# Kernel optimization log

Measured on AMD Instinct MI355X. Metric: run time of the kernel, lower is better.

## Reference

```python
import jax, jax.numpy as jnp
import numpy as np

B, C_IN, C_OUT, H, W, K = 8, 32, 32, 96, 96, 5


def setup_inputs() -> dict:
    key = jax.random.key(0)
    k1, k2 = jax.random.split(key)
    f = jax.random.normal(k1, (B, C_IN, H, W), dtype=jnp.float32)
    # xavier_uniform-style init for the structuring element h
    fan_in = C_IN * K * K
    fan_out = C_OUT * K * K
    bound = float(np.sqrt(6.0 / (fan_in + fan_out)))
    h = jax.random.uniform(k2, (C_OUT, C_IN, K, K), dtype=jnp.float32,
                           minval=-bound, maxval=bound)
    return {"f": f, "h": h}


def reference(f, h):
    """Morphological max-plus dilation with 'same' padding.

    out[b,o,y,x] = max_{c,i,j} f[b,c,y+i-p, x+j-p] + h[o,c,i,j]
    """
    b, c, hh, ww = f.shape
    o, _, k, _ = h.shape
    p = k // 2
    neg = -jnp.finfo(f.dtype).max / 2
    fp = jnp.pad(f, ((0, 0), (0, 0), (p, p), (p, p)), constant_values=neg)
    out = jnp.full((b, o, hh, ww), neg, dtype=f.dtype)
    for i in range(k):          # fixed small kernel loop (k*k = 25 taps)
        for j in range(k):
            sl = fp[:, :, i:i + hh, j:j + ww]              # (B, C, H, W)
            w_ij = h[:, :, i, j]                            # (O, C)
            # max-plus over input channels: (B,1,C,H,W) + (O,C,1,1)
            cand = jnp.max(sl[:, None] + w_ij[None, :, :, None, None], axis=2)
            out = jnp.maximum(out, cand)
    return out
```

## Files before the change

kernel.cpp:

```cpp
#include <hip/hip_runtime.h>


#define B_ 8
#define C_ 32
#define O_ 32
#define H_ 96
#define W_ 96
#define K_ 5
#define KK_ (K_ * K_)

#define TX_ 24
#define RT_ 4
#define CS_ 4
#define TY_ (RT_ * CS_)
#define NT_ (TX_ * TY_)
#define XR_ 4
#define OP_ 2
#define OB_ (OP_ * 2)
#define CG_ (C_ / CS_)

#define PH_ 100
#define PW_ 104
#define PLSZ_ (PH_ * PW_)
#define FPAD_BYTES ((size_t)B_ * C_ * PLSZ_ * 4)

#define NEGF (-30000.0f)

typedef _Float16 h2 __attribute__((ext_vector_type(2)));

static __device__ __forceinline__ h2 h2b(unsigned u) {
    return __builtin_bit_cast(h2, u);
}
static __device__ __forceinline__ unsigned bh2(h2 v) {
    return __builtin_bit_cast(unsigned, v);
}

__global__ __launch_bounds__(256)
void prepad_kernel(const float* __restrict__ f, unsigned* __restrict__ fpad) {
    const int idx = blockIdx.x * 256 + threadIdx.x;
    const int c = blockIdx.y;
    const int b = blockIdx.z;
    if (idx >= PLSZ_) return;
    const int row = idx / PW_;
    const int col = idx - row * PW_;
    const int y = row - 2;
    const int x = col - 2;
    float v = NEGF;
    if ((unsigned)y < H_ && (unsigned)x < W_)
        v = f[((size_t)(b * C_ + c) * H_ + y) * W_ + x];
    _Float16 hv = (_Float16)v;
    h2 d; d.x = hv; d.y = hv;
    fpad[(size_t)(b * C_ + c) * PLSZ_ + idx] = bh2(d);
}

template <bool PADDED>
__global__ __launch_bounds__(NT_)
void dilate_main(const unsigned* __restrict__ fpad,
                 const float* __restrict__ f,
                 const float* __restrict__ h, float* __restrict__ out) {
    const int tx  = threadIdx.x;
    const int ty  = threadIdx.y;
    const int tid = ty * TX_ + tx;
    const int ry  = ty & (RT_ - 1);
    const int g   = ty >> 2;

    const int ytile = blockIdx.x;
    const int og    = blockIdx.y;
    const int b     = blockIdx.z;
    const int y0 = ytile * RT_;
    const int o0 = og * OB_;
    const int x0 = XR_ * tx;
    const int yb = y0 + ry;

    __shared__ unsigned hs2[C_][64];
    __shared__ unsigned comb[CS_ - 1][OP_ * XR_][RT_ * TX_];

    for (int idx = tid; idx < C_ * KK_ * OP_; idx += NT_) {
        int c  = idx / (KK_ * OP_);
        int rr = idx - c * (KK_ * OP_);
        int ij = rr / OP_;
        int op = rr - ij * OP_;
        int o  = o0 + 2 * op;
        float a0 = h[((size_t)o * C_ + c) * KK_ + ij];
        float a1 = h[((size_t)(o + 1) * C_ + c) * KK_ + ij];
        h2 p; p.x = (_Float16)a0; p.y = (_Float16)a1;
        hs2[c][ij * OP_ + op] = bh2(p);
    }
    __syncthreads();

    h2 acc[OP_][XR_];
    {
        h2 neg; neg.x = (_Float16)NEGF; neg.y = (_Float16)NEGF;
#pragma unroll
        for (int op = 0; op < OP_; ++op)
#pragma unroll
            for (int xx = 0; xx < XR_; ++xx) acc[op][xx] = neg;
    }

    const int c0 = g * CG_;
    for (int cc = 0; cc < CG_; ++cc) {
        const int c = c0 + cc;

        unsigned win[K_][8];
        if (PADDED) {
            const unsigned* p =
                fpad + (size_t)(b * C_ + c) * PLSZ_ + yb * PW_ + x0;
#pragma unroll
            for (int i = 0; i < K_; ++i) {
                const uint4* q = (const uint4*)(p + i * PW_);
                uint4 w0 = q[0];
                uint4 w1 = q[1];
                win[i][0] = w0.x; win[i][1] = w0.y;
                win[i][2] = w0.z; win[i][3] = w0.w;
                win[i][4] = w1.x; win[i][5] = w1.y;
                win[i][6] = w1.z; win[i][7] = w1.w;
            }
        } else {
            const float* fc = f + (size_t)(b * C_ + c) * (H_ * W_);
#pragma unroll
            for (int i = 0; i < K_; ++i) {
#pragma unroll
                for (int q = 0; q < 8; ++q) {
                    int yy = yb + i - 2;
                    int xc = x0 - 2 + q;
                    bool ok = ((unsigned)yy < H_) && ((unsigned)xc < W_);
                    float v = ok ? fc[(size_t)yy * W_ + xc] : NEGF;
                    _Float16 hv = (_Float16)v;
                    h2 d; d.x = hv; d.y = hv;
                    win[i][q] = bh2(d);
                }
            }
        }

        unsigned hu[2 * KK_];
        {
            const uint4* hsrc = (const uint4*)&hs2[c][0];
#pragma unroll
            for (int k = 0; k < 12; ++k) {
                uint4 v = hsrc[k];
                hu[4 * k]     = v.x;
                hu[4 * k + 1] = v.y;
                hu[4 * k + 2] = v.z;
                hu[4 * k + 3] = v.w;
            }
            uint2 hd = *(const uint2*)&hs2[c][48];
            hu[48] = hd.x;
            hu[49] = hd.y;
        }

#pragma unroll
        for (int n = 0; n < 2 * KK_; ++n) asm volatile("" : "+v"(hu[n]));
#pragma unroll
        for (int i = 0; i < K_; ++i)
#pragma unroll
            for (int q = 0; q < 8; ++q) asm volatile("" : "+v"(win[i][q]));

#pragma unroll
        for (int i = 0; i < K_; ++i) {
#pragma unroll
            for (int j = 0; j < K_; ++j) {
                h2 h0 = h2b(hu[(i * K_ + j) * OP_]);
                h2 h1 = h2b(hu[(i * K_ + j) * OP_ + 1]);
#pragma unroll
                for (int xx = 0; xx < XR_; ++xx) {
                    h2 fv = h2b(win[i][xx + j]);
                    acc[0][xx] = __builtin_elementwise_max(acc[0][xx], fv + h0);
                    acc[1][xx] = __builtin_elementwise_max(acc[1][xx], fv + h1);
                }
            }
        }
    }

    const int t96 = ry * TX_ + tx;
    if (g > 0) {
#pragma unroll
        for (int op = 0; op < OP_; ++op)
#pragma unroll
            for (int xx = 0; xx < XR_; ++xx)
                comb[g - 1][op * XR_ + xx][t96] = bh2(acc[op][xx]);
    }
    __syncthreads();
    if (g == 0) {
#pragma unroll
        for (int op = 0; op < OP_; ++op)
#pragma unroll
            for (int xx = 0; xx < XR_; ++xx) {
                const int row = op * XR_ + xx;
                h2 v0 = h2b(comb[0][row][t96]);
                h2 v1 = h2b(comb[1][row][t96]);
                h2 v2 = h2b(comb[2][row][t96]);
                h2 m = __builtin_elementwise_max(v0, v1);
                m = __builtin_elementwise_max(m, v2);
                acc[op][xx] = __builtin_elementwise_max(acc[op][xx], m);
            }

        const int y = yb;
#pragma unroll
        for (int op = 0; op < OP_; ++op) {
            const int o = o0 + 2 * op;
            float4 lo = make_float4((float)acc[op][0].x, (float)acc[op][1].x,
                                    (float)acc[op][2].x, (float)acc[op][3].x);
            float4 hi = make_float4((float)acc[op][0].y, (float)acc[op][1].y,
                                    (float)acc[op][2].y, (float)acc[op][3].y);
            *(float4*)&out[(((size_t)b * O_ + o)     * H_ + y) * W_ + x0] = lo;
            *(float4*)&out[(((size_t)b * O_ + o + 1) * H_ + y) * W_ + x0] = hi;
        }
    }
}

extern "C" void kernel_launch(void* const* d_in, const int* in_sizes, int n_in,
                              void* d_out, int out_size, void* d_ws, size_t ws_size,
                              hipStream_t stream) {
    const float* f = (const float*)d_in[0];
    const float* h = (const float*)d_in[1];
    float* out = (float*)d_out;

    dim3 mgrid(H_ / RT_, O_ / OB_, B_);
    dim3 mblock(TX_, TY_);

    if (ws_size >= FPAD_BYTES) {
        unsigned* fpad = (unsigned*)d_ws;
        dim3 pgrid((PLSZ_ + 255) / 256, C_, B_);
        hipLaunchKernelGGL(prepad_kernel, pgrid, dim3(256), 0, stream, f, fpad);
        hipLaunchKernelGGL((dilate_main<true>), mgrid, mblock, 0, stream,
                           fpad, f, h, out);
    } else {
        hipLaunchKernelGGL((dilate_main<false>), mgrid, mblock, 0, stream,
                           (const unsigned*)nullptr, f, h, out);
    }
}
```

Measured before the change: 150.4 us.

## Pack channel pairs into half2 lanes instead of output-channel pairs

Changes the packed fp16 layout so each half2 lane holds two input channels rather than two output channels, halving the prepadded input buffer and the per-block channel loop count. Each thread now accumulates four output channels, reading weights from shared memory per tap rather than preloading them into registers, and folds the two lanes with a final fmax. The add and max are issued through inline asm for packed f16 ops. This removes the duplicated broadcast of input values across lanes and halves global window loads, at the cost of more accumulator registers and more LDS weight reads inside the inner loop.

```diff
diff --git a/kernel.cpp b/kernel.cpp
--- a/kernel.cpp
+++ b/kernel.cpp
@@ -8,6 +8,7 @@
 #define W_ 96
 #define K_ 5
 #define KK_ (K_ * K_)
+#define NCP_ (C_ / 2)
 
 #define TX_ 24
 #define RT_ 4
@@ -15,14 +16,13 @@
 #define TY_ (RT_ * CS_)
 #define NT_ (TX_ * TY_)
 #define XR_ 4
-#define OP_ 2
-#define OB_ (OP_ * 2)
-#define CG_ (C_ / CS_)
+#define OB_ 4
+#define CPG_ (NCP_ / CS_)
 
 #define PH_ 100
 #define PW_ 104
 #define PLSZ_ (PH_ * PW_)
-#define FPAD_BYTES ((size_t)B_ * C_ * PLSZ_ * 4)
+#define FPAD_BYTES ((size_t)B_ * NCP_ * PLSZ_ * 4)
 
 #define NEGF (-30000.0f)
 
@@ -33,24 +33,31 @@
 }
 static __device__ __forceinline__ unsigned bh2(h2 v) {
     return __builtin_bit_cast(unsigned, v);
+}
+
+static __device__ __forceinline__ void pk_addmax(h2& acc, h2 fv, h2 hv) {
+    h2 t;
+    asm("v_pk_add_f16 %0, %1, %2" : "=v"(t) : "v"(fv), "v"(hv));
+    asm("v_pk_max_f16 %0, %1, %2" : "=v"(acc) : "v"(acc), "v"(t));
 }
 
 __global__ __launch_bounds__(256)
 void prepad_kernel(const float* __restrict__ f, unsigned* __restrict__ fpad) {
     const int idx = blockIdx.x * 256 + threadIdx.x;
-    const int c = blockIdx.y;
-    const int b = blockIdx.z;
+    const int cp = blockIdx.y;
+    const int b  = blockIdx.z;
     if (idx >= PLSZ_) return;
     const int row = idx / PW_;
     const int col = idx - row * PW_;
     const int y = row - 2;
     const int x = col - 2;
-    float v = NEGF;
-    if ((unsigned)y < H_ && (unsigned)x < W_)
-        v = f[((size_t)(b * C_ + c) * H_ + y) * W_ + x];
-    _Float16 hv = (_Float16)v;
-    h2 d; d.x = hv; d.y = hv;
-    fpad[(size_t)(b * C_ + c) * PLSZ_ + idx] = bh2(d);
+    float v0 = NEGF, v1 = NEGF;
+    if ((unsigned)y < H_ && (unsigned)x < W_) {
+        v0 = f[((size_t)(b * C_ + 2 * cp)     * H_ + y) * W_ + x];
+        v1 = f[((size_t)(b * C_ + 2 * cp + 1) * H_ + y) * W_ + x];
+    }
+    h2 d; d.x = (_Float16)v0; d.y = (_Float16)v1;
+    fpad[(size_t)(b * NCP_ + cp) * PLSZ_ + idx] = bh2(d);
 }
 
 template <bool PADDED>
@@ -72,51 +79,51 @@
     const int x0 = XR_ * tx;
     const int yb = y0 + ry;
 
-    __shared__ unsigned hs2[C_][64];
-    __shared__ unsigned comb[CS_ - 1][OP_ * XR_][RT_ * TX_];
-
-    for (int idx = tid; idx < C_ * KK_ * OP_; idx += NT_) {
-        int c  = idx / (KK_ * OP_);
-        int rr = idx - c * (KK_ * OP_);
-        int ij = rr / OP_;
-        int op = rr - ij * OP_;
-        int o  = o0 + 2 * op;
-        float a0 = h[((size_t)o * C_ + c) * KK_ + ij];
-        float a1 = h[((size_t)(o + 1) * C_ + c) * KK_ + ij];
+    __shared__ unsigned hs2[NCP_][104];
+    __shared__ unsigned comb[CS_ - 1][OB_ * XR_][RT_ * TX_];
+
+    for (int idx = tid; idx < NCP_ * KK_ * OB_; idx += NT_) {
+        int cp = idx / (KK_ * OB_);
+        int rr = idx - cp * (KK_ * OB_);
+        int ij = rr / OB_;
+        int o  = rr - ij * OB_;
+        float a0 = h[((size_t)(o0 + o) * C_ + 2 * cp)     * KK_ + ij];
+        float a1 = h[((size_t)(o0 + o) * C_ + 2 * cp + 1) * KK_ + ij];
         h2 p; p.x = (_Float16)a0; p.y = (_Float16)a1;
-        hs2[c][ij * OP_ + op] = bh2(p);
+        hs2[cp][ij * OB_ + o] = bh2(p);
     }
     __syncthreads();
 
-    h2 acc[OP_][XR_];
+    h2 acc[OB_][XR_];
     {
         h2 neg; neg.x = (_Float16)NEGF; neg.y = (_Float16)NEGF;
 #pragma unroll
-        for (int op = 0; op < OP_; ++op)
-#pragma unroll
-            for (int xx = 0; xx < XR_; ++xx) acc[op][xx] = neg;
-    }
-
-    const int c0 = g * CG_;
-    for (int cc = 0; cc < CG_; ++cc) {
-        const int c = c0 + cc;
-
-        unsigned win[K_][8];
+        for (int o = 0; o < OB_; ++o)
+#pragma unroll
+            for (int xx = 0; xx < XR_; ++xx) acc[o][xx] = neg;
+    }
+
+    const int cp0 = g * CPG_;
+    for (int cpi = 0; cpi < CPG_; ++cpi) {
+        const int cp = cp0 + cpi;
+
+        h2 win[K_][8];
         if (PADDED) {
             const unsigned* p =
-                fpad + (size_t)(b * C_ + c) * PLSZ_ + yb * PW_ + x0;
+                fpad + (size_t)(b * NCP_ + cp) * PLSZ_ + yb * PW_ + x0;
 #pragma unroll
             for (int i = 0; i < K_; ++i) {
                 const uint4* q = (const uint4*)(p + i * PW_);
                 uint4 w0 = q[0];
                 uint4 w1 = q[1];
-                win[i][0] = w0.x; win[i][1] = w0.y;
-                win[i][2] = w0.z; win[i][3] = w0.w;
-                win[i][4] = w1.x; win[i][5] = w1.y;
-                win[i][6] = w1.z; win[i][7] = w1.w;
+                win[i][0] = h2b(w0.x); win[i][1] = h2b(w0.y);
+                win[i][2] = h2b(w0.z); win[i][3] = h2b(w0.w);
+                win[i][4] = h2b(w1.x); win[i][5] = h2b(w1.y);
+                win[i][6] = h2b(w1.z); win[i][7] = h2b(w1.w);
             }
         } else {
-            const float* fc = f + (size_t)(b * C_ + c) * (H_ * W_);
+            const float* fc0 = f + (size_t)(b * C_ + 2 * cp) * (H_ * W_);
+            const float* fc1 = f + (size_t)(b * C_ + 2 * cp + 1) * (H_ * W_);
 #pragma unroll
             for (int i = 0; i < K_; ++i) {
 #pragma unroll
@@ -124,48 +131,28 @@
                     int yy = yb + i - 2;
                     int xc = x0 - 2 + q;
                     bool ok = ((unsigned)yy < H_) && ((unsigned)xc < W_);
-                    float v = ok ? fc[(size_t)yy * W_ + xc] : NEGF;
-                    _Float16 hv = (_Float16)v;
-                    h2 d; d.x = hv; d.y = hv;
-                    win[i][q] = bh2(d);
+                    float v0 = ok ? fc0[(size_t)yy * W_ + xc] : NEGF;
+                    float v1 = ok ? fc1[(size_t)yy * W_ + xc] : NEGF;
+                    h2 d; d.x = (_Float16)v0; d.y = (_Float16)v1;
+                    win[i][q] = d;
                 }
             }
         }
 
-        unsigned hu[2 * KK_];
-        {
-            const uint4* hsrc = (const uint4*)&hs2[c][0];
-#pragma unroll
-            for (int k = 0; k < 12; ++k) {
-                uint4 v = hsrc[k];
-                hu[4 * k]     = v.x;
-                hu[4 * k + 1] = v.y;
-                hu[4 * k + 2] = v.z;
-                hu[4 * k + 3] = v.w;
-            }
-            uint2 hd = *(const uint2*)&hs2[c][48];
-            hu[48] = hd.x;
-            hu[49] = hd.y;
-        }
-
-#pragma unroll
-        for (int n = 0; n < 2 * KK_; ++n) asm volatile("" : "+v"(hu[n]));
-#pragma unroll
-        for (int i = 0; i < K_; ++i)
-#pragma unroll
-            for (int q = 0; q < 8; ++q) asm volatile("" : "+v"(win[i][q]));
-
 #pragma unroll
         for (int i = 0; i < K_; ++i) {
 #pragma unroll
             for (int j = 0; j < K_; ++j) {
-                h2 h0 = h2b(hu[(i * K_ + j) * OP_]);
-                h2 h1 = h2b(hu[(i * K_ + j) * OP_ + 1]);
+                uint4 hq = *(const uint4*)&hs2[cp][(i * K_ + j) * OB_];
+                h2 h0 = h2b(hq.x), h1 = h2b(hq.y);
+                h2 h02 = h2b(hq.z), h3 = h2b(hq.w);
 #pragma unroll
                 for (int xx = 0; xx < XR_; ++xx) {
-                    h2 fv = h2b(win[i][xx + j]);
-                    acc[0][xx] = __builtin_elementwise_max(acc[0][xx], fv + h0);
-                    acc[1][xx] = __builtin_elementwise_max(acc[1][xx], fv + h1);
+                    h2 fv = win[i][xx + j];
+                    pk_addmax(acc[0][xx], fv, h0);
+                    pk_addmax(acc[1][xx], fv, h1);
+                    pk_addmax(acc[2][xx], fv, h02);
+                    pk_addmax(acc[3][xx], fv, h3);
                 }
             }
         }
@@ -174,36 +161,35 @@
     const int t96 = ry * TX_ + tx;
     if (g > 0) {
 #pragma unroll
-        for (int op = 0; op < OP_; ++op)
+        for (int o = 0; o < OB_; ++o)
 #pragma unroll
             for (int xx = 0; xx < XR_; ++xx)
-                comb[g - 1][op * XR_ + xx][t96] = bh2(acc[op][xx]);
+                comb[g - 1][o * XR_ + xx][t96] = bh2(acc[o][xx]);
     }
     __syncthreads();
     if (g == 0) {
 #pragma unroll
-        for (int op = 0; op < OP_; ++op)
+        for (int o = 0; o < OB_; ++o)
 #pragma unroll
             for (int xx = 0; xx < XR_; ++xx) {
-                const int row = op * XR_ + xx;
+                const int row = o * XR_ + xx;
                 h2 v0 = h2b(comb[0][row][t96]);
                 h2 v1 = h2b(comb[1][row][t96]);
                 h2 v2 = h2b(comb[2][row][t96]);
                 h2 m = __builtin_elementwise_max(v0, v1);
                 m = __builtin_elementwise_max(m, v2);
-                acc[op][xx] = __builtin_elementwise_max(acc[op][xx], m);
+                acc[o][xx] = __builtin_elementwise_max(acc[o][xx], m);
             }
 
         const int y = yb;
 #pragma unroll
-        for (int op = 0; op < OP_; ++op) {
-            const int o = o0 + 2 * op;
-            float4 lo = make_float4((float)acc[op][0].x, (float)acc[op][1].x,
-                                    (float)acc[op][2].x, (float)acc[op][3].x);
-            float4 hi = make_float4((float)acc[op][0].y, (float)acc[op][1].y,
-                                    (float)acc[op][2].y, (float)acc[op][3].y);
-            *(float4*)&out[(((size_t)b * O_ + o)     * H_ + y) * W_ + x0] = lo;
-            *(float4*)&out[(((size_t)b * O_ + o + 1) * H_ + y) * W_ + x0] = hi;
+        for (int o = 0; o < OB_; ++o) {
+            float r[XR_];
+#pragma unroll
+            for (int xx = 0; xx < XR_; ++xx)
+                r[xx] = fmaxf((float)acc[o][xx].x, (float)acc[o][xx].y);
+            float4 v = make_float4(r[0], r[1], r[2], r[3]);
+            *(float4*)&out[(((size_t)b * O_ + (o0 + o)) * H_ + y) * W_ + x0] = v;
         }
     }
 }
@@ -220,7 +206,7 @@
 
     if (ws_size >= FPAD_BYTES) {
         unsigned* fpad = (unsigned*)d_ws;
-        dim3 pgrid((PLSZ_ + 255) / 256, C_, B_);
+        dim3 pgrid((PLSZ_ + 255) / 256, NCP_, B_);
         hipLaunchKernelGGL(prepad_kernel, pgrid, dim3(256), 0, stream, f, fpad);
         hipLaunchKernelGGL((dilate_main<true>), mgrid, mblock, 0, stream,
                            fpad, f, h, out);
```

New measurement: 144.5 us. 1.04x faster.
